# Kernel optimization log

Hardware: AMD Instinct MI355X
Metric: run time of the kernel (lower is better)

## Reference

```python
import jax, jax.numpy as jnp
import numpy as np

HID = 128

def _gru_cell(xt, hx, w_ih, w_hh, b_ih, b_hh):
    # PyTorch GRUCell: gates ordered r, z, n along dim 0 of weights
    gi = xt @ w_ih.T + b_ih          # [n, 3H]
    gh = hx @ w_hh.T + b_hh          # [n, 3H]
    i_r, i_z, i_n = jnp.split(gi, 3, axis=-1)
    h_r, h_z, h_n = jnp.split(gh, 3, axis=-1)
    r = jax.nn.sigmoid(i_r + h_r)
    z = jax.nn.sigmoid(i_z + h_z)
    n_ = jnp.tanh(i_n + r * h_n)
    return (1.0 - z) * n_ + z * hx


def setup_inputs() -> dict:
    key = jax.random.key(0)
    ks = jax.random.split(key, 11)
    n = 32768
    s = 0.05
    return {
        "x": jax.random.normal(ks[0], (n, 1, 28, 28), jnp.float32),
        "w_ih1": jax.random.normal(ks[1], (3 * HID, 28), jnp.float32) * s,
        "w_hh1": jax.random.normal(ks[2], (3 * HID, HID), jnp.float32) * s,
        "b_ih1": jax.random.normal(ks[3], (3 * HID,), jnp.float32) * s,
        "b_hh1": jax.random.normal(ks[4], (3 * HID,), jnp.float32) * s,
        "w_ih2": jax.random.normal(ks[5], (3 * HID, HID), jnp.float32) * s,
        "w_hh2": jax.random.normal(ks[6], (3 * HID, HID), jnp.float32) * s,
        "b_ih2": jax.random.normal(ks[7], (3 * HID,), jnp.float32) * s,
        "b_hh2": jax.random.normal(ks[8], (3 * HID,), jnp.float32) * s,
        "w_out": jax.random.normal(ks[9], (10, HID), jnp.float32) * s,
        "b_out": jax.random.normal(ks[10], (10,), jnp.float32) * s,
    }


def reference(x, w_ih1, w_hh1, b_ih1, b_hh1, w_ih2, w_hh2, b_ih2, b_hh2, w_out, b_out):
    n, c, h, w = x.shape
    xs = x.transpose(0, 2, 3, 1).reshape(n, h, w * c)   # [n, 28, 28]
    xs_t = jnp.swapaxes(xs, 0, 1)                       # [h, n, 28] for scan
    h0 = jnp.zeros((n, HID), x.dtype)

    def step(carry, xt):
        h1, h2 = carry
        h1 = jax.nn.relu(_gru_cell(xt, h1, w_ih1, w_hh1, b_ih1, b_hh1))
        h2 = jax.nn.relu(_gru_cell(h1, h2, w_ih2, w_hh2, b_ih2, b_hh2))
        return (h1, h2), None

    (h1, h2), _ = jax.lax.scan(step, (h0, h0), xs_t)
    return h2 @ w_out.T + b_out                         # [n, 10]
```

## Files before the change

### kernel.cpp

```cpp
#include <hip/hip_runtime.h>

typedef _Float16 f16;
typedef _Float16 f16x8 __attribute__((ext_vector_type(8)));
typedef float f32x4 __attribute__((ext_vector_type(4)));

#define NROWS 32768
#define BR 32
#define TS 28

#define MFMA16(A, B, C) __builtin_amdgcn_mfma_f32_16x16x32_f16((A), (B), (C), 0, 0, 0)

__device__ __forceinline__ f32x4 splat4(float v) { f32x4 r = {v, v, v, v}; return r; }
__device__ __forceinline__ float frcp(float v) { return __builtin_amdgcn_rcpf(v); }
__device__ __forceinline__ float fsig(float v) { return frcp(1.f + __expf(-v)); }
__device__ __forceinline__ float ftanh(float v) {
  float e = __expf(v + v);
  return 1.f - 2.f * frcp(e + 1.f);
}

__global__ void prep_weights(const float* __restrict__ wih1,
                             const float* __restrict__ whh1,
                             const float* __restrict__ wih2,
                             const float* __restrict__ whh2,
                             f16* __restrict__ wsf) {
  const int f = blockIdx.x;
  const int lane = threadIdx.x;
  const float* src;
  int K, nt, kt;
  if (f < 24)       { src = wih1; K = 28;  nt = f;             kt = 0; }
  else if (f < 120) { src = whh1; K = 128; int i = f - 24;  nt = i >> 2; kt = i & 3; }
  else if (f < 216) { src = wih2; K = 128; int i = f - 120; nt = i >> 2; kt = i & 3; }
  else              { src = whh2; K = 128; int i = f - 216; nt = i >> 2; kt = i & 3; }
  const int n  = nt * 16 + (lane & 15);
  const int k0 = kt * 32 + (lane >> 4) * 8;
  f16x8 pack;
#pragma unroll
  for (int i = 0; i < 8; i++) {
    const int k = k0 + i;
    float v = (k < K) ? src[n * K + k] : 0.f;
    pack[i] = (f16)v;
  }
  ((f16x8*)wsf)[f * 64 + lane] = pack;
}

__global__ __launch_bounds__(512, 2) void gru_main(
    const float* __restrict__ x,
    const float* __restrict__ bih1, const float* __restrict__ bhh1,
    const float* __restrict__ bih2, const float* __restrict__ bhh2,
    const float* __restrict__ wout, const float* __restrict__ bout,
    const f16* __restrict__ wsf,
    float* __restrict__ out) {
  __shared__ __align__(16) f16 h1b[2][BR * 128];
  __shared__ __align__(16) f16 h2b[2][BR * 128];
  __shared__ __align__(16) f16 wsh1[96 * 512];
  __shared__ __align__(16) f16 wshx[24 * 512];

  const int tid  = threadIdx.x;
  const int wv   = tid >> 6;
  const int lane = tid & 63;
  const int lr   = lane & 15;
  const int kg   = lane >> 4;
  const int row0 = blockIdx.x * BR;
  const int d    = wv * 16 + lr;
  const int sw   = (lr & 7) << 3;

  const f16x8* wf = (const f16x8*)wsf;

  {
    f16x8* wd1 = (f16x8*)wsh1;
    const f16x8* ws1 = wf + 24 * 64;
#pragma unroll
    for (int i = 0; i < 12; i++) wd1[tid + 512 * i] = ws1[tid + 512 * i];
    f16x8* wdx = (f16x8*)wshx;
#pragma unroll
    for (int i = 0; i < 3; i++) wdx[tid + 512 * i] = wf[tid + 512 * i];
    unsigned int* z1 = (unsigned int*)&h1b[0][0];
    unsigned int* z2 = (unsigned int*)&h2b[1][0];
#pragma unroll
    for (int i = 0; i < 4; i++) { z1[tid + 512 * i] = 0u; z2[tid + 512 * i] = 0u; }
  }

  f16x8 Wih2[3][4], Whh2[3][4];
#pragma unroll
  for (int g = 0; g < 3; g++) {
    const int nt = wv + g * 8;
#pragma unroll
    for (int kt = 0; kt < 4; kt++) {
      Wih2[g][kt] = wf[(120 + nt * 4 + kt) * 64 + lane];
      Whh2[g][kt] = wf[(216 + nt * 4 + kt) * 64 + lane];
    }
  }

  const float b1r = bih1[d] + bhh1[d];
  const float b1z = bih1[128 + d] + bhh1[128 + d];
  const float b1i = bih1[256 + d];
  const float b1h = bhh1[256 + d];
  const float b2r = bih2[d] + bhh2[d];
  const float b2z = bih2[128 + d] + bhh2[128 + d];
  const float b2i = bih2[256 + d];
  const float b2h = bhh2[256 + d];

  float h1s[2][4] = {{0, 0, 0, 0}, {0, 0, 0, 0}};
  float h2s[2][4] = {{0, 0, 0, 0}, {0, 0, 0, 0}};

  const float* xp0 = x + (size_t)(row0 + lr) * 784 + kg * 8;
  const float* xp1 = xp0 + (size_t)16 * 784;

  const f16x8* wl1 = (const f16x8*)wsh1;
  const f16x8* wlx = (const f16x8*)wshx;

  __syncthreads();

  auto phase = [&](int p, bool L1, bool L2) {
    const int cur = p & 1;
    const f16* h1r = h1b[cur];
    const f16* h2r = h2b[cur];
    f16* h1w = h1b[cur ^ 1];
    f16* h2w = h2b[cur ^ 1];

    float4 q00, q01, q10, q11;
    if (L1) {
      const float* a = xp0 + p * 28;
      const float* b = xp1 + p * 28;
      q00 = *(const float4*)a;
      q10 = *(const float4*)b;
      float4 zz = {0.f, 0.f, 0.f, 0.f};
      q01 = zz; q11 = zz;
      if (kg < 3) { q01 = *(const float4*)(a + 4); q11 = *(const float4*)(b + 4); }
    }

    f32x4 aR1[2], aZ1[2], aI1[2], aH1[2];
    f32x4 aR2[2], aZ2[2], aI2[2], aH2[2];
    if (L1) {
#pragma unroll
      for (int rt = 0; rt < 2; rt++) {
        aR1[rt] = splat4(b1r); aZ1[rt] = splat4(b1z);
        aI1[rt] = splat4(b1i); aH1[rt] = splat4(b1h);
      }
    }
    if (L2) {
#pragma unroll
      for (int rt = 0; rt < 2; rt++) {
        aR2[rt] = splat4(b2r); aZ2[rt] = splat4(b2z);
        aI2[rt] = splat4(b2i); aH2[rt] = splat4(b2h);
      }
    }

#pragma unroll
    for (int kt = 0; kt < 4; kt++) {
      const int o0 = (lr * 128 + kt * 32 + kg * 8) ^ sw;
      const int o1 = ((16 + lr) * 128 + kt * 32 + kg * 8) ^ sw;
      f16x8 a10 = *(const f16x8*)&h1r[o0];
      f16x8 a11 = *(const f16x8*)&h1r[o1];
      if (L1) {
        f16x8 w0 = wl1[((wv     ) * 4 + kt) * 64 + lane];
        f16x8 w1 = wl1[((wv +  8) * 4 + kt) * 64 + lane];
        f16x8 w2 = wl1[((wv + 16) * 4 + kt) * 64 + lane];
        aR1[0] = MFMA16(a10, w0, aR1[0]); aR1[1] = MFMA16(a11, w0, aR1[1]);
        aZ1[0] = MFMA16(a10, w1, aZ1[0]); aZ1[1] = MFMA16(a11, w1, aZ1[1]);
        aH1[0] = MFMA16(a10, w2, aH1[0]); aH1[1] = MFMA16(a11, w2, aH1[1]);
      }
      if (L2) {
        f16x8 a20 = *(const f16x8*)&h2r[o0];
        f16x8 a21 = *(const f16x8*)&h2r[o1];
        aR2[0] = MFMA16(a10, Wih2[0][kt], aR2[0]); aR2[1] = MFMA16(a11, Wih2[0][kt], aR2[1]);
        aZ2[0] = MFMA16(a10, Wih2[1][kt], aZ2[0]); aZ2[1] = MFMA16(a11, Wih2[1][kt], aZ2[1]);
        aI2[0] = MFMA16(a10, Wih2[2][kt], aI2[0]); aI2[1] = MFMA16(a11, Wih2[2][kt], aI2[1]);
        aR2[0] = MFMA16(a20, Whh2[0][kt], aR2[0]); aR2[1] = MFMA16(a21, Whh2[0][kt], aR2[1]);
        aZ2[0] = MFMA16(a20, Whh2[1][kt], aZ2[0]); aZ2[1] = MFMA16(a21, Whh2[1][kt], aZ2[1]);
        aH2[0] = MFMA16(a20, Whh2[2][kt], aH2[0]); aH2[1] = MFMA16(a21, Whh2[2][kt], aH2[1]);
      }
    }

    if (L1) {
      f16x8 ax0, ax1;
      ax0[0] = (f16)q00.x; ax0[1] = (f16)q00.y; ax0[2] = (f16)q00.z; ax0[3] = (f16)q00.w;
      ax0[4] = (f16)q01.x; ax0[5] = (f16)q01.y; ax0[6] = (f16)q01.z; ax0[7] = (f16)q01.w;
      ax1[0] = (f16)q10.x; ax1[1] = (f16)q10.y; ax1[2] = (f16)q10.z; ax1[3] = (f16)q10.w;
      ax1[4] = (f16)q11.x; ax1[5] = (f16)q11.y; ax1[6] = (f16)q11.z; ax1[7] = (f16)q11.w;
      f16x8 u0 = wlx[(wv     ) * 64 + lane];
      f16x8 u1 = wlx[(wv +  8) * 64 + lane];
      f16x8 u2 = wlx[(wv + 16) * 64 + lane];
      aR1[0] = MFMA16(ax0, u0, aR1[0]); aR1[1] = MFMA16(ax1, u0, aR1[1]);
      aZ1[0] = MFMA16(ax0, u1, aZ1[0]); aZ1[1] = MFMA16(ax1, u1, aZ1[1]);
      aI1[0] = MFMA16(ax0, u2, aI1[0]); aI1[1] = MFMA16(ax1, u2, aI1[1]);
    }

    if (L2) {
#pragma unroll
      for (int rt = 0; rt < 2; rt++) {
#pragma unroll
        for (int i = 0; i < 4; i++) {
          float rg = fsig(aR2[rt][i]);
          float zg = fsig(aZ2[rt][i]);
          float nn = ftanh(fmaf(rg, aH2[rt][i], aI2[rt][i]));
          float hp = h2s[rt][i];
          float hn = fmaxf(fmaf(zg, hp - nn, nn), 0.f);
          h2s[rt][i] = hn;
          const int rr = rt * 16 + kg * 4 + i;
          h2w[(rr * 128 + d) ^ ((rr & 7) << 3)] = (f16)hn;
        }
      }
    }
    if (L1) {
#pragma unroll
      for (int rt = 0; rt < 2; rt++) {
#pragma unroll
        for (int i = 0; i < 4; i++) {
          float rg = fsig(aR1[rt][i]);
          float zg = fsig(aZ1[rt][i]);
          float nn = ftanh(fmaf(rg, aH1[rt][i], aI1[rt][i]));
          float hp = h1s[rt][i];
          float hn = fmaxf(fmaf(zg, hp - nn, nn), 0.f);
          h1s[rt][i] = hn;
          const int rr = rt * 16 + kg * 4 + i;
          h1w[(rr * 128 + d) ^ ((rr & 7) << 3)] = (f16)hn;
        }
      }
    }
    __syncthreads();
  };

  phase(0, true, false);
  for (int p = 1; p < TS; p++) phase(p, true, true);
  phase(TS, false, true);

  const int orow = tid >> 4;
  const int ocol = tid & 15;
  if (ocol < 10) {
    const f16* hb = h2b[1];
    float s = bout[ocol];
#pragma unroll 8
    for (int k = 0; k < 128; k++) {
      float hv = (float)hb[(orow * 128 + k) ^ ((orow & 7) << 3)];
      s = fmaf(hv, wout[ocol * 128 + k], s);
    }
    out[(size_t)(row0 + orow) * 10 + ocol] = s;
  }
}

extern "C" void kernel_launch(void* const* d_in, const int* in_sizes, int n_in,
                              void* d_out, int out_size, void* d_ws, size_t ws_size,
                              hipStream_t stream) {
  const float* x    = (const float*)d_in[0];
  const float* wih1 = (const float*)d_in[1];
  const float* whh1 = (const float*)d_in[2];
  const float* bih1 = (const float*)d_in[3];
  const float* bhh1 = (const float*)d_in[4];
  const float* wih2 = (const float*)d_in[5];
  const float* whh2 = (const float*)d_in[6];
  const float* bih2 = (const float*)d_in[7];
  const float* bhh2 = (const float*)d_in[8];
  const float* wout = (const float*)d_in[9];
  const float* bout = (const float*)d_in[10];
  f16* wsf   = (f16*)d_ws;
  float* out = (float*)d_out;

  prep_weights<<<312, 64, 0, stream>>>(wih1, whh1, wih2, whh2, wsf);
  gru_main<<<NROWS / BR, 512, 0, stream>>>(x, bih1, bhh1, bih2, bhh2,
                                           wout, bout, wsf, out);
}
```

Baseline: 613.9 us.

## Split GRU layers across two wave groups in 1024-thread blocks

Doubles the block to 1024 threads and gives each layer its own group of 8 waves. Group 0 computes layer 1 with W_hh1 in registers and W_ih1 in LDS, while group 1 computes layer 2 with W_hh2 in registers and W_ih2 staged in LDS, pipelined one timestep apart. This splits MFMA and gate work across more waves and lowers per-thread register pressure. In exchange the launch bounds change, the two groups do unequal work so one may idle at each barrier, and LDS usage per block is similar, which may limit blocks per CU.

```diff
diff --git a/kernel.cpp b/kernel.cpp
--- a/kernel.cpp
+++ b/kernel.cpp
@@ -43,7 +43,7 @@
   ((f16x8*)wsf)[f * 64 + lane] = pack;
 }
 
-__global__ __launch_bounds__(512, 2) void gru_main(
+__global__ __launch_bounds__(1024, 4) void gru_main(
     const float* __restrict__ x,
     const float* __restrict__ bih1, const float* __restrict__ bhh1,
     const float* __restrict__ bih2, const float* __restrict__ bhh2,
@@ -52,11 +52,13 @@
     float* __restrict__ out) {
   __shared__ __align__(16) f16 h1b[2][BR * 128];
   __shared__ __align__(16) f16 h2b[2][BR * 128];
-  __shared__ __align__(16) f16 wsh1[96 * 512];
   __shared__ __align__(16) f16 wshx[24 * 512];
+  __shared__ __align__(16) f16 wsh2[96 * 512];
 
   const int tid  = threadIdx.x;
-  const int wv   = tid >> 6;
+  const int wid  = tid >> 6;
+  const int grp  = wid >> 3;
+  const int wv   = wid & 7;
   const int lane = tid & 63;
   const int lr   = lane & 15;
   const int kg   = lane >> 4;
@@ -67,167 +69,135 @@
   const f16x8* wf = (const f16x8*)wsf;
 
   {
-    f16x8* wd1 = (f16x8*)wsh1;
-    const f16x8* ws1 = wf + 24 * 64;
-#pragma unroll
-    for (int i = 0; i < 12; i++) wd1[tid + 512 * i] = ws1[tid + 512 * i];
     f16x8* wdx = (f16x8*)wshx;
-#pragma unroll
-    for (int i = 0; i < 3; i++) wdx[tid + 512 * i] = wf[tid + 512 * i];
+    if (tid < 512) wdx[1024 + tid] = wf[1024 + tid];
+    wdx[tid] = wf[tid];
+    f16x8* wd2 = (f16x8*)wsh2;
+    const f16x8* ws2 = wf + 120 * 64;
+#pragma unroll
+    for (int i = 0; i < 6; i++) wd2[tid + 1024 * i] = ws2[tid + 1024 * i];
     unsigned int* z1 = (unsigned int*)&h1b[0][0];
     unsigned int* z2 = (unsigned int*)&h2b[1][0];
-#pragma unroll
-    for (int i = 0; i < 4; i++) { z1[tid + 512 * i] = 0u; z2[tid + 512 * i] = 0u; }
-  }
-
-  f16x8 Wih2[3][4], Whh2[3][4];
-#pragma unroll
-  for (int g = 0; g < 3; g++) {
-    const int nt = wv + g * 8;
-#pragma unroll
-    for (int kt = 0; kt < 4; kt++) {
-      Wih2[g][kt] = wf[(120 + nt * 4 + kt) * 64 + lane];
-      Whh2[g][kt] = wf[(216 + nt * 4 + kt) * 64 + lane];
-    }
-  }
-
-  const float b1r = bih1[d] + bhh1[d];
-  const float b1z = bih1[128 + d] + bhh1[128 + d];
-  const float b1i = bih1[256 + d];
-  const float b1h = bhh1[256 + d];
-  const float b2r = bih2[d] + bhh2[d];
-  const float b2z = bih2[128 + d] + bhh2[128 + d];
-  const float b2i = bih2[256 + d];
-  const float b2h = bhh2[256 + d];
-
-  float h1s[2][4] = {{0, 0, 0, 0}, {0, 0, 0, 0}};
-  float h2s[2][4] = {{0, 0, 0, 0}, {0, 0, 0, 0}};
-
-  const float* xp0 = x + (size_t)(row0 + lr) * 784 + kg * 8;
-  const float* xp1 = xp0 + (size_t)16 * 784;
-
-  const f16x8* wl1 = (const f16x8*)wsh1;
+    z1[tid] = 0u; z1[tid + 1024] = 0u;
+    z2[tid] = 0u; z2[tid + 1024] = 0u;
+  }
+
+  const int wbase = grp ? 216 : 24;
+  f16x8 Wreg[3][4];
+#pragma unroll
+  for (int g = 0; g < 3; g++)
+#pragma unroll
+    for (int kt = 0; kt < 4; kt++)
+      Wreg[g][kt] = wf[(wbase + (wv + g * 8) * 4 + kt) * 64 + lane];
+
+  const float* bi = grp ? bih2 : bih1;
+  const float* bh = grp ? bhh2 : bhh1;
+  const float br_ = bi[d] + bh[d];
+  const float bz_ = bi[128 + d] + bh[128 + d];
+  const float bin = bi[256 + d];
+  const float bhn = bh[256 + d];
+
+  float hs[2][4] = {{0, 0, 0, 0}, {0, 0, 0, 0}};
+
   const f16x8* wlx = (const f16x8*)wshx;
+  const f16x8* wl2 = (const f16x8*)wsh2;
 
   __syncthreads();
 
-  auto phase = [&](int p, bool L1, bool L2) {
+  for (int p = 0; p <= TS; p++) {
     const int cur = p & 1;
     const f16* h1r = h1b[cur];
+    f16* h1w = h1b[cur ^ 1];
     const f16* h2r = h2b[cur];
-    f16* h1w = h1b[cur ^ 1];
     f16* h2w = h2b[cur ^ 1];
 
-    float4 q00, q01, q10, q11;
-    if (L1) {
-      const float* a = xp0 + p * 28;
-      const float* b = xp1 + p * 28;
-      q00 = *(const float4*)a;
-      q10 = *(const float4*)b;
-      float4 zz = {0.f, 0.f, 0.f, 0.f};
-      q01 = zz; q11 = zz;
-      if (kg < 3) { q01 = *(const float4*)(a + 4); q11 = *(const float4*)(b + 4); }
-    }
-
-    f32x4 aR1[2], aZ1[2], aI1[2], aH1[2];
-    f32x4 aR2[2], aZ2[2], aI2[2], aH2[2];
-    if (L1) {
-#pragma unroll
-      for (int rt = 0; rt < 2; rt++) {
-        aR1[rt] = splat4(b1r); aZ1[rt] = splat4(b1z);
-        aI1[rt] = splat4(b1i); aH1[rt] = splat4(b1h);
-      }
-    }
-    if (L2) {
-#pragma unroll
-      for (int rt = 0; rt < 2; rt++) {
-        aR2[rt] = splat4(b2r); aZ2[rt] = splat4(b2z);
-        aI2[rt] = splat4(b2i); aH2[rt] = splat4(b2h);
-      }
-    }
-
-#pragma unroll
-    for (int kt = 0; kt < 4; kt++) {
-      const int o0 = (lr * 128 + kt * 32 + kg * 8) ^ sw;
-      const int o1 = ((16 + lr) * 128 + kt * 32 + kg * 8) ^ sw;
-      f16x8 a10 = *(const f16x8*)&h1r[o0];
-      f16x8 a11 = *(const f16x8*)&h1r[o1];
-      if (L1) {
-        f16x8 w0 = wl1[((wv     ) * 4 + kt) * 64 + lane];
-        f16x8 w1 = wl1[((wv +  8) * 4 + kt) * 64 + lane];
-        f16x8 w2 = wl1[((wv + 16) * 4 + kt) * 64 + lane];
-        aR1[0] = MFMA16(a10, w0, aR1[0]); aR1[1] = MFMA16(a11, w0, aR1[1]);
-        aZ1[0] = MFMA16(a10, w1, aZ1[0]); aZ1[1] = MFMA16(a11, w1, aZ1[1]);
-        aH1[0] = MFMA16(a10, w2, aH1[0]); aH1[1] = MFMA16(a11, w2, aH1[1]);
-      }
-      if (L2) {
-        f16x8 a20 = *(const f16x8*)&h2r[o0];
-        f16x8 a21 = *(const f16x8*)&h2r[o1];
-        aR2[0] = MFMA16(a10, Wih2[0][kt], aR2[0]); aR2[1] = MFMA16(a11, Wih2[0][kt], aR2[1]);
-        aZ2[0] = MFMA16(a10, Wih2[1][kt], aZ2[0]); aZ2[1] = MFMA16(a11, Wih2[1][kt], aZ2[1]);
-        aI2[0] = MFMA16(a10, Wih2[2][kt], aI2[0]); aI2[1] = MFMA16(a11, Wih2[2][kt], aI2[1]);
-        aR2[0] = MFMA16(a20, Whh2[0][kt], aR2[0]); aR2[1] = MFMA16(a21, Whh2[0][kt], aR2[1]);
-        aZ2[0] = MFMA16(a20, Whh2[1][kt], aZ2[0]); aZ2[1] = MFMA16(a21, Whh2[1][kt], aZ2[1]);
-        aH2[0] = MFMA16(a20, Whh2[2][kt], aH2[0]); aH2[1] = MFMA16(a21, Whh2[2][kt], aH2[1]);
-      }
-    }
-
-    if (L1) {
-      f16x8 ax0, ax1;
-      ax0[0] = (f16)q00.x; ax0[1] = (f16)q00.y; ax0[2] = (f16)q00.z; ax0[3] = (f16)q00.w;
-      ax0[4] = (f16)q01.x; ax0[5] = (f16)q01.y; ax0[6] = (f16)q01.z; ax0[7] = (f16)q01.w;
-      ax1[0] = (f16)q10.x; ax1[1] = (f16)q10.y; ax1[2] = (f16)q10.z; ax1[3] = (f16)q10.w;
-      ax1[4] = (f16)q11.x; ax1[5] = (f16)q11.y; ax1[6] = (f16)q11.z; ax1[7] = (f16)q11.w;
-      f16x8 u0 = wlx[(wv     ) * 64 + lane];
-      f16x8 u1 = wlx[(wv +  8) * 64 + lane];
-      f16x8 u2 = wlx[(wv + 16) * 64 + lane];
-      aR1[0] = MFMA16(ax0, u0, aR1[0]); aR1[1] = MFMA16(ax1, u0, aR1[1]);
-      aZ1[0] = MFMA16(ax0, u1, aZ1[0]); aZ1[1] = MFMA16(ax1, u1, aZ1[1]);
-      aI1[0] = MFMA16(ax0, u2, aI1[0]); aI1[1] = MFMA16(ax1, u2, aI1[1]);
-    }
-
-    if (L2) {
-#pragma unroll
-      for (int rt = 0; rt < 2; rt++) {
-#pragma unroll
-        for (int i = 0; i < 4; i++) {
-          float rg = fsig(aR2[rt][i]);
-          float zg = fsig(aZ2[rt][i]);
-          float nn = ftanh(fmaf(rg, aH2[rt][i], aI2[rt][i]));
-          float hp = h2s[rt][i];
-          float hn = fmaxf(fmaf(zg, hp - nn, nn), 0.f);
-          h2s[rt][i] = hn;
-          const int rr = rt * 16 + kg * 4 + i;
-          h2w[(rr * 128 + d) ^ ((rr & 7) << 3)] = (f16)hn;
+    if (grp == 0) {
+      if (p < TS) {
+        float4 q[2][2];
+#pragma unroll
+        for (int rt = 0; rt < 2; rt++) {
+          const float* a = x + (size_t)(row0 + rt * 16 + lr) * 784 + p * 28 + kg * 8;
+          q[rt][0] = *(const float4*)a;
+          float4 zz = {0.f, 0.f, 0.f, 0.f};
+          q[rt][1] = zz;
+          if (kg < 3) q[rt][1] = *(const float4*)(a + 4);
+        }
+#pragma unroll
+        for (int rt = 0; rt < 2; rt++) {
+          f32x4 aR = splat4(br_), aZ = splat4(bz_), aI = splat4(bin), aH = splat4(bhn);
+          const int ro = (rt * 16 + lr) * 128;
+#pragma unroll
+          for (int kt = 0; kt < 4; kt++) {
+            f16x8 a1 = *(const f16x8*)&h1r[(ro + kt * 32 + kg * 8) ^ sw];
+            aR = MFMA16(a1, Wreg[0][kt], aR);
+            aZ = MFMA16(a1, Wreg[1][kt], aZ);
+            aH = MFMA16(a1, Wreg[2][kt], aH);
+          }
+          f16x8 ax;
+          ax[0] = (f16)q[rt][0].x; ax[1] = (f16)q[rt][0].y;
+          ax[2] = (f16)q[rt][0].z; ax[3] = (f16)q[rt][0].w;
+          ax[4] = (f16)q[rt][1].x; ax[5] = (f16)q[rt][1].y;
+          ax[6] = (f16)q[rt][1].z; ax[7] = (f16)q[rt][1].w;
+          f16x8 u0 = wlx[(wv     ) * 64 + lane];
+          f16x8 u1 = wlx[(wv +  8) * 64 + lane];
+          f16x8 u2 = wlx[(wv + 16) * 64 + lane];
+          aR = MFMA16(ax, u0, aR);
+          aZ = MFMA16(ax, u1, aZ);
+          aI = MFMA16(ax, u2, aI);
+#pragma unroll
+          for (int i = 0; i < 4; i++) {
+            float rg = fsig(aR[i]);
+            float zg = fsig(aZ[i]);
+            float nn = ftanh(fmaf(rg, aH[i], aI[i]));
+            float hp = hs[rt][i];
+            float hn = fmaxf(fmaf(zg, hp - nn, nn), 0.f);
+            hs[rt][i] = hn;
+            const int rr = rt * 16 + kg * 4 + i;
+            h1w[(rr * 128 + d) ^ ((rr & 7) << 3)] = (f16)hn;
+          }
         }
       }
-    }
-    if (L1) {
-#pragma unroll
-      for (int rt = 0; rt < 2; rt++) {
-#pragma unroll
-        for (int i = 0; i < 4; i++) {
-          float rg = fsig(aR1[rt][i]);
-          float zg = fsig(aZ1[rt][i]);
-          float nn = ftanh(fmaf(rg, aH1[rt][i], aI1[rt][i]));
-          float hp = h1s[rt][i];
-          float hn = fmaxf(fmaf(zg, hp - nn, nn), 0.f);
-          h1s[rt][i] = hn;
-          const int rr = rt * 16 + kg * 4 + i;
-          h1w[(rr * 128 + d) ^ ((rr & 7) << 3)] = (f16)hn;
+    } else {
+      if (p >= 1) {
+#pragma unroll
+        for (int rt = 0; rt < 2; rt++) {
+          f32x4 aR = splat4(br_), aZ = splat4(bz_), aI = splat4(bin), aH = splat4(bhn);
+          const int ro = (rt * 16 + lr) * 128;
+#pragma unroll
+          for (int kt = 0; kt < 4; kt++) {
+            const int o = (ro + kt * 32 + kg * 8) ^ sw;
+            f16x8 a1 = *(const f16x8*)&h1r[o];
+            f16x8 a2 = *(const f16x8*)&h2r[o];
+            f16x8 u0 = wl2[((wv     ) * 4 + kt) * 64 + lane];
+            f16x8 u1 = wl2[((wv +  8) * 4 + kt) * 64 + lane];
+            f16x8 u2 = wl2[((wv + 16) * 4 + kt) * 64 + lane];
+            aR = MFMA16(a1, u0, aR);
+            aZ = MFMA16(a1, u1, aZ);
+            aI = MFMA16(a1, u2, aI);
+            aR = MFMA16(a2, Wreg[0][kt], aR);
+            aZ = MFMA16(a2, Wreg[1][kt], aZ);
+            aH = MFMA16(a2, Wreg[2][kt], aH);
+          }
+#pragma unroll
+          for (int i = 0; i < 4; i++) {
+            float rg = fsig(aR[i]);
+            float zg = fsig(aZ[i]);
+            float nn = ftanh(fmaf(rg, aH[i], aI[i]));
+            float hp = hs[rt][i];
+            float hn = fmaxf(fmaf(zg, hp - nn, nn), 0.f);
+            hs[rt][i] = hn;
+            const int rr = rt * 16 + kg * 4 + i;
+            h2w[(rr * 128 + d) ^ ((rr & 7) << 3)] = (f16)hn;
+          }
         }
       }
     }
     __syncthreads();
-  };
-
-  phase(0, true, false);
-  for (int p = 1; p < TS; p++) phase(p, true, true);
-  phase(TS, false, true);
+  }
 
   const int orow = tid >> 4;
   const int ocol = tid & 15;
-  if (ocol < 10) {
+  if (orow < BR && ocol < 10) {
     const f16* hb = h2b[1];
     float s = bout[ocol];
 #pragma unroll 8
@@ -257,6 +227,6 @@
   float* out = (float*)d_out;
 
   prep_weights<<<312, 64, 0, stream>>>(wih1, whh1, wih2, whh2, wsf);
-  gru_main<<<NROWS / BR, 512, 0, stream>>>(x, bih1, bhh1, bih2, bhh2,
-                                           wout, bout, wsf, out);
-}
+  gru_main<<<NROWS / BR, 1024, 0, stream>>>(x, bih1, bhh1, bih2, bhh2,
+                                            wout, bout, wsf, out);
+}
```

New measurement: 593.0 us. 3.4% less time.
